# Kernel optimization log

Hardware: AMD Instinct MI355X
Metric: run time of the kernel (lower is better)

Reference implementation:

```python
import jax, jax.numpy as jnp
import numpy as np

HEADS = 16
DIM_HEAD = 64
SCALE = DIM_HEAD ** -0.5


def setup_inputs() -> dict:
    key = jax.random.key(0)
    k1, k2, k3 = jax.random.split(key, 3)
    B, N, C = 2, 2048, 1024
    inner = HEADS * DIM_HEAD  # 1024
    x = jax.random.normal(k1, (B, N, C), dtype=jnp.float32)
    w_qkv = jax.random.normal(k2, (C, 3 * inner), dtype=jnp.float32) * (C ** -0.5)
    w_proj = jax.random.normal(k3, (inner, C), dtype=jnp.float32) * (inner ** -0.5)
    b_proj = jnp.zeros((C,), dtype=jnp.float32)
    return {"x": x, "w_qkv": w_qkv, "w_proj": w_proj, "b_proj": b_proj}


def reference(x, w_qkv, w_proj, b_proj):
    B, N, C = x.shape
    qkv = x @ w_qkv  # [B, N, 3*inner]
    qkv = qkv.reshape(B, N, 3, HEADS, DIM_HEAD)
    qkv = jnp.transpose(qkv, (2, 0, 3, 1, 4))  # [3, B, H, N, D]
    q, k, v = qkv[0], qkv[1], qkv[2]
    q = q * SCALE
    attn = jnp.einsum('bhnd,bhmd->bhnm', q, k)  # [B, H, N, N]
    attn = jax.nn.softmax(attn, axis=-1)
    out = jnp.einsum('bhnm,bhmd->bhnd', attn, v)  # [B, H, N, D]
    out = jnp.transpose(out, (0, 2, 1, 3)).reshape(B, N, HEADS * DIM_HEAD)
    return out @ w_proj + b_proj
```

## Files before the change

### kernel.cpp

```cpp
#include <hip/hip_runtime.h>
#include <hip/hip_bf16.h>
#include <cstdint>
#include <cstddef>

static constexpr int BATCH = 2;
static constexpr int SEQ   = 2048;
static constexpr int CDIM  = 1024;
static constexpr int ROWS  = BATCH * SEQ;
static constexpr int QKVN  = 3 * CDIM;
static constexpr int QKN   = 2 * CDIM;

typedef short bf16x8 __attribute__((ext_vector_type(8)));
typedef short bf16x4 __attribute__((ext_vector_type(4)));
typedef float f32x4  __attribute__((ext_vector_type(4)));

__device__ inline short f2bf(float f) {
    union { float f; unsigned u; } v; v.f = f;
    unsigned u = v.u;
    u += 0x7fffu + ((u >> 16) & 1u);
    return (short)(u >> 16);
}

__device__ inline unsigned pk_bf16(float a, float b) {
#if __has_builtin(__builtin_amdgcn_cvt_pk_bf16_f32)
    auto r = __builtin_amdgcn_cvt_pk_bf16_f32(a, b);
    return __builtin_bit_cast(unsigned, r);
#else
    union { float f; unsigned u; } ua, ub;
    ua.f = a; ub.f = b;
    unsigned xa = ua.u + 0x7fffu + ((ua.u >> 16) & 1u);
    unsigned xb = ub.u + 0x7fffu + ((ub.u >> 16) & 1u);
    return __builtin_amdgcn_perm(xb, xa, 0x07060302);
#endif
}

__device__ inline void glds16(const short* g, short* l) {
    __builtin_amdgcn_global_load_lds(
        (const __attribute__((address_space(1))) void*)g,
        (__attribute__((address_space(3))) void*)l, 16, 0, 0);
}

__device__ inline f32x4 mfma16_bf16(bf16x4 a, bf16x4 b, f32x4 c) {
#if __has_builtin(__builtin_amdgcn_mfma_f32_16x16x16bf16_1k)
    return __builtin_amdgcn_mfma_f32_16x16x16bf16_1k(a, b, c, 0, 0, 0);
#else
    asm("v_mfma_f32_16x16x16_bf16 %0, %1, %2, %0" : "+v"(c) : "v"(a), "v"(b));
    return c;
#endif
}

__device__ inline int swz_src(int lane) {
    return ((lane & 3) ^ ((lane >> 3) & 3)) * 8;
}
__device__ inline int swz_rd(int quad, int l15) {
    return (quad ^ ((l15 >> 1) & 3)) * 8;
}

__global__ __launch_bounds__(256) void prep(const float* __restrict__ x,
                                            const float* __restrict__ wqkv,
                                            const float* __restrict__ wproj,
                                            short* __restrict__ x_bf,
                                            short* __restrict__ wqkvT,
                                            short* __restrict__ wprojT,
                                            float smul) {
    __shared__ float tile[32][33];
    const int bid = blockIdx.x, t = threadIdx.x;
    if (bid < 4096) {
        int i = bid * 256 + t;
        float4 f = ((const float4*)x)[i];
        uint2 o;
        o.x = pk_bf16(f.x, f.y);
        o.y = pk_bf16(f.z, f.w);
        ((uint2*)x_bf)[i] = o;
        return;
    }
    const float* in; short* out; int C, r0, c0; float scale; int srows;
    if (bid < 7168) {
        int b2 = bid - 4096;
        in = wqkv; out = wqkvT; C = QKVN;
        c0 = (b2 % 96) * 32; r0 = (b2 / 96) * 32;
        scale = smul; srows = 1024;
    } else {
        int b3 = bid - 7168;
        in = wproj; out = wprojT; C = CDIM;
        c0 = (b3 & 31) * 32; r0 = (b3 >> 5) * 32;
        scale = 1.0f; srows = 0;
    }
    int tx = t & 31, ty = t >> 5;
    #pragma unroll
    for (int i = 0; i < 4; i++)
        tile[ty + i * 8][tx] = in[(size_t)(r0 + ty + i * 8) * C + c0 + tx];
    __syncthreads();
    #pragma unroll
    for (int i = 0; i < 4; i++) {
        int orow = c0 + ty + i * 8;
        float sc = (orow < srows) ? scale : 1.0f;
        out[(size_t)orow * CDIM + r0 + tx] = f2bf(tile[tx][ty + i * 8] * sc);
    }
}

template<int BF16OUT, int MT>
__device__ __forceinline__ void gemm_core(const short* __restrict__ A,
                                          const short* __restrict__ Bt,
                                          void* __restrict__ C,
                                          const float* __restrict__ bias,
                                          int N, int K, int m0, int n0,
                                          short* As, short* Bs) {
    constexpr int AF = MT / 32;
    constexpr int APAN = MT * 32;
    constexpr int BPAN = 128 * 32;
    const int t = threadIdx.x, wave = t >> 6, lane = t & 63;
    const int l15 = lane & 15, quad = lane >> 4;
    const int wr = wave >> 1, wc = wave & 1;
    const int sg = swz_src(lane);
    const int rsl = swz_rd(quad, l15);

    f32x4 acc[AF][4] = {};

    const short* gA = A  + (size_t)(m0 + wave * (MT / 4) + (lane >> 2)) * K + sg;
    const short* gB = Bt + (size_t)(n0 + wave * 32 + (lane >> 2)) * K + sg;
    short* lA = &As[wave * (MT / 4) * 32];
    short* lB = &Bs[wave * 32 * 32];

    for (int k0 = 0; k0 < K; k0 += 64) {
        glds16(gA + k0,      lA);
        glds16(gA + k0 + 32, lA + APAN);
        if constexpr (MT == 128) {
            glds16(gA + 16 * K + k0,      lA + 512);
            glds16(gA + 16 * K + k0 + 32, lA + APAN + 512);
        }
        glds16(gB + k0,               lB);
        glds16(gB + 16 * K + k0,      lB + 512);
        glds16(gB + k0 + 32,          lB + BPAN);
        glds16(gB + 16 * K + k0 + 32, lB + BPAN + 512);
        __syncthreads();

        #pragma unroll
        for (int st = 0; st < 2; st++) {
            bf16x8 af[AF], bfv[4];
            #pragma unroll
            for (int i = 0; i < AF; i++)
                af[i] = *(const bf16x8*)&As[st * APAN + (wr * (MT / 2) + i * 16 + l15) * 32 + rsl];
            #pragma unroll
            for (int j = 0; j < 4; j++)
                bfv[j] = *(const bf16x8*)&Bs[st * BPAN + (wc * 64 + j * 16 + l15) * 32 + rsl];
            #pragma unroll
            for (int i = 0; i < AF; i++)
                #pragma unroll
                for (int j = 0; j < 4; j++)
                    acc[i][j] = __builtin_amdgcn_mfma_f32_16x16x32_bf16(af[i], bfv[j], acc[i][j], 0, 0, 0);
        }
        __syncthreads();
    }

    #pragma unroll
    for (int i = 0; i < AF; i++) {
        #pragma unroll
        for (int j = 0; j < 4; j++) {
            #pragma unroll
            for (int r = 0; r < 4; r++) {
                int row = m0 + wr * (MT / 2) + i * 16 + quad * 4 + r;
                int col = n0 + wc * 64 + j * 16 + l15;
                float v = acc[i][j][r];
                if (BF16OUT) ((short*)C)[(size_t)row * N + col] = f2bf(v);
                else         ((float*)C)[(size_t)row * N + col] = v + bias[col];
            }
        }
    }
}

__global__ __launch_bounds__(256) void gemm_qk_v(const short* __restrict__ x_bf,
                                                 const short* __restrict__ wqkvT,
                                                 short* __restrict__ qk,
                                                 short* __restrict__ vT) {
    __shared__ __align__(16) short As[128 * 64];
    __shared__ __align__(16) short Bs[128 * 64];
    const int bid = blockIdx.x;
    if (bid < 512) {
        gemm_core<1, 128>(x_bf, wqkvT, qk, nullptr, QKN, CDIM,
                          (bid >> 4) * 128, (bid & 15) * 128, As, Bs);
    } else {
        int b2 = bid - 512;
        gemm_core<1, 128>(wqkvT + (size_t)QKN * CDIM, x_bf, vT, nullptr, ROWS, CDIM,
                          (b2 >> 5) * 128, (b2 & 31) * 128, As, Bs);
    }
}

__global__ __launch_bounds__(256) void gemm_proj(const short* __restrict__ A,
                                                 const short* __restrict__ Bt,
                                                 float* __restrict__ C,
                                                 const float* __restrict__ bias) {
    __shared__ __align__(16) short As[64 * 64];
    __shared__ __align__(16) short Bs[128 * 64];
    gemm_core<0, 64>(A, Bt, C, bias, CDIM, CDIM,
                     blockIdx.y * 64, blockIdx.x * 128, As, Bs);
}

static constexpr int KBUF  = 2 * 128 * 32;
static constexpr int VOFF  = 2 * KBUF;
static constexpr int LDV   = 136;
static constexpr int VBUF  = 64 * LDV;
static constexpr int SMEM_SH = VOFF + 2 * VBUF;

__global__ __launch_bounds__(512) void attn_kernel(const short* __restrict__ qk,
                                                   const short* __restrict__ vTg,
                                                   short* __restrict__ attn_out) {
    __shared__ __align__(16) short smem[SMEM_SH];

    const int t = threadIdx.x, wave = t >> 6, lane = t & 63;
    const int l15 = lane & 15, quad = lane >> 4;
    const int g = wave >> 2, wl = wave & 3;
    const int lid = blockIdx.x;
    const int bh = (lid & 7) * 4 + (lid >> 7);
    const int q0 = ((lid >> 3) & 15) * 128;
    const int b = bh >> 4, h = bh & 15;
    const size_t baseQ = (size_t)(b * SEQ) * QKN + h * 64;
    const int rsl = swz_rd(quad, l15);

    const size_t qoff0 = baseQ + (size_t)(q0 + wl * 32 + l15) * QKN + quad * 8;
    const size_t qoff1 = qoff0 + (size_t)16 * QKN;
    bf16x8 qf00 = *(const bf16x8*)&qk[qoff0];
    bf16x8 qf01 = *(const bf16x8*)&qk[qoff0 + 32];
    bf16x8 qf10 = *(const bf16x8*)&qk[qoff1];
    bf16x8 qf11 = *(const bf16x8*)&qk[qoff1 + 32];

    const short* gK = qk + baseQ + 1024
                    + (size_t)(wave * 16 + (lane >> 2)) * QKN + swz_src(lane);
    const short* gV = vTg + (size_t)(h * 64) * ROWS + b * SEQ;
    const int vd = t >> 3, vc = t & 7;

    const bf16x4 ones = { (short)0x3F80, (short)0x3F80, (short)0x3F80, (short)0x3F80 };

    f32x4 ot0[4] = {}, ot1[4] = {};
    f32x4 ol0 = {}, ol1 = {};

    glds16(gK,      smem + wave * 512);
    glds16(gK + 32, smem + 4096 + wave * 512);
    {
        int4 va = *(const int4*)&gV[(size_t)vd * ROWS + vc * 8];
        int4 vb = *(const int4*)&gV[(size_t)vd * ROWS + 64 + vc * 8];
        *(int4*)&smem[VOFF + vd * LDV + vc * 8]      = va;
        *(int4*)&smem[VOFF + vd * LDV + 64 + vc * 8] = vb;
    }

    for (int j = 0; j < SEQ / 128; j++) {
        const int cur = j & 1, nxt = cur ^ 1;
        __syncthreads();

        int4 va, vb;
        if (j < SEQ / 128 - 1) {
            const size_t jadd = (size_t)(j + 1) * 128 * QKN;
            short* kb = smem + nxt * KBUF + wave * 512;
            glds16(gK + jadd,      kb);
            glds16(gK + jadd + 32, kb + 4096);
            va = *(const int4*)&gV[(size_t)vd * ROWS + (j + 1) * 128 + vc * 8];
            vb = *(const int4*)&gV[(size_t)vd * ROWS + (j + 1) * 128 + 64 + vc * 8];
        }

        const short* Kb0 = smem + cur * KBUF;
        const short* Kb1 = Kb0 + 4096;
        const short* Vb  = smem + VOFF + cur * VBUF;

        #pragma unroll
        for (int sub = 0; sub < 4; sub++) {
            const int gsub = g * 4 + sub;
            bf16x8 kf0 = *(const bf16x8*)&Kb0[(gsub * 16 + l15) * 32 + rsl];
            bf16x8 kf1 = *(const bf16x8*)&Kb1[(gsub * 16 + l15) * 32 + rsl];
            f32x4 a0 = {}, a1 = {};
            __builtin_amdgcn_s_setprio(1);
            a0 = __builtin_amdgcn_mfma_f32_16x16x32_bf16(kf0, qf00, a0, 0, 0, 0);
            a0 = __builtin_amdgcn_mfma_f32_16x16x32_bf16(kf1, qf01, a0, 0, 0, 0);
            a1 = __builtin_amdgcn_mfma_f32_16x16x32_bf16(kf0, qf10, a1, 0, 0, 0);
            a1 = __builtin_amdgcn_mfma_f32_16x16x32_bf16(kf1, qf11, a1, 0, 0, 0);
            __builtin_amdgcn_s_setprio(0);
            union { unsigned u[2]; bf16x4 v; } pu0, pu1;
            pu0.u[0] = pk_bf16(__builtin_amdgcn_exp2f(a0[0]), __builtin_amdgcn_exp2f(a0[1]));
            pu0.u[1] = pk_bf16(__builtin_amdgcn_exp2f(a0[2]), __builtin_amdgcn_exp2f(a0[3]));
            pu1.u[0] = pk_bf16(__builtin_amdgcn_exp2f(a1[0]), __builtin_amdgcn_exp2f(a1[1]));
            pu1.u[1] = pk_bf16(__builtin_amdgcn_exp2f(a1[2]), __builtin_amdgcn_exp2f(a1[3]));
            __builtin_amdgcn_s_setprio(1);
            ol0 = mfma16_bf16(ones, pu0.v, ol0);
            ol1 = mfma16_bf16(ones, pu1.v, ol1);
            #pragma unroll
            for (int d = 0; d < 4; d++) {
                bf16x4 vf = *(const bf16x4*)&Vb[(d * 16 + l15) * LDV + gsub * 16 + quad * 4];
                ot0[d] = mfma16_bf16(vf, pu0.v, ot0[d]);
                ot1[d] = mfma16_bf16(vf, pu1.v, ot1[d]);
            }
            __builtin_amdgcn_s_setprio(0);
        }

        if (j < SEQ / 128 - 1) {
            *(int4*)&smem[VOFF + nxt * VBUF + vd * LDV + vc * 8]      = va;
            *(int4*)&smem[VOFF + nxt * VBUF + vd * LDV + 64 + vc * 8] = vb;
        }
    }

    __syncthreads();
    float* pf   = (float*)smem;
    float* lbuf = (float*)smem + 128 * 68;
    short* tr   = smem + 18432;

    if (g == 1) {
        #pragma unroll
        for (int d = 0; d < 4; d++) {
            #pragma unroll
            for (int r = 0; r < 4; r++) {
                pf[(wl * 32 + l15) * 68      + d * 16 + quad * 4 + r] = ot0[d][r];
                pf[(wl * 32 + 16 + l15) * 68 + d * 16 + quad * 4 + r] = ot1[d][r];
            }
        }
        lbuf[wl * 32 + l15]      = ol0[0];
        lbuf[wl * 32 + 16 + l15] = ol1[0];
    }
    __syncthreads();
    if (g == 0) {
        float inv0 = 1.0f / (ol0[0] + lbuf[wl * 32 + l15]);
        float inv1 = 1.0f / (ol1[0] + lbuf[wl * 32 + 16 + l15]);
        #pragma unroll
        for (int d = 0; d < 4; d++) {
            int pb0 = (wl * 32 + l15) * 68      + d * 16 + quad * 4;
            int pb1 = (wl * 32 + 16 + l15) * 68 + d * 16 + quad * 4;
            float c00 = (ot0[d][0] + pf[pb0 + 0]) * inv0;
            float c01 = (ot0[d][1] + pf[pb0 + 1]) * inv0;
            float c02 = (ot0[d][2] + pf[pb0 + 2]) * inv0;
            float c03 = (ot0[d][3] + pf[pb0 + 3]) * inv0;
            float c10 = (ot1[d][0] + pf[pb1 + 0]) * inv1;
            float c11 = (ot1[d][1] + pf[pb1 + 1]) * inv1;
            float c12 = (ot1[d][2] + pf[pb1 + 2]) * inv1;
            float c13 = (ot1[d][3] + pf[pb1 + 3]) * inv1;
            int o0 = (wl * 32 + l15) * 72 + d * 16 + quad * 4;
            int o1 = (wl * 32 + 16 + l15) * 72 + d * 16 + quad * 4;
            *(unsigned*)&tr[o0]     = pk_bf16(c00, c01);
            *(unsigned*)&tr[o0 + 2] = pk_bf16(c02, c03);
            *(unsigned*)&tr[o1]     = pk_bf16(c10, c11);
            *(unsigned*)&tr[o1 + 2] = pk_bf16(c12, c13);
        }
    }
    __syncthreads();
    {
        int row = t >> 2, c4 = t & 3;
        #pragma unroll
        for (int p = 0; p < 2; p++) {
            int ch = c4 * 2 + p;
            int4 v = *(const int4*)&tr[row * 72 + ch * 8];
            *(int4*)&attn_out[(size_t)(b * SEQ + q0 + row) * CDIM + h * 64 + ch * 8] = v;
        }
    }
}

extern "C" void kernel_launch(void* const* d_in, const int* in_sizes, int n_in,
                              void* d_out, int out_size, void* d_ws, size_t ws_size,
                              hipStream_t stream) {
    const float* x      = (const float*)d_in[0];
    const float* w_qkv  = (const float*)d_in[1];
    const float* w_proj = (const float*)d_in[2];
    const float* b_proj = (const float*)d_in[3];
    float* out = (float*)d_out;

    char* ws = (char*)d_ws;
    short* x_bf    = (short*)(ws);
    short* wqkvT   = (short*)(ws + 8388608);
    short* wprojT  = (short*)(ws + 14680064);
    short* qk_bf   = (short*)(ws + 16777216);
    short* vTg     = (short*)(ws + 33554432);
    short* attn_bf = (short*)(ws + 41943040);

    const float SMUL = 0.125f * 1.44269504088896340736f;

    prep<<<8192, 256, 0, stream>>>(x, w_qkv, w_proj, x_bf, wqkvT, wprojT, SMUL);

    gemm_qk_v<<<768, 256, 0, stream>>>(x_bf, wqkvT, qk_bf, vTg);

    attn_kernel<<<dim3(512), 512, 0, stream>>>(qk_bf, vTg, attn_bf);

    gemm_proj<<<dim3(CDIM / 128, ROWS / 64), 256, 0, stream>>>(attn_bf, wprojT, out, b_proj);
}
```

Baseline: 181.6 us.

## Single-buffer V tile in LDS to shrink attention shared memory

Replaces the double-buffered V tile with a single V buffer and packs the epilogue scratch (row sums stored in a padding column of the partial-output buffer) so the kernel's shared memory drops to 26624 shorts. The intent is to fit more 512-thread blocks per CU and raise occupancy. In exchange, each iteration now needs an extra barrier before overwriting V and another after writing it, which adds synchronisation stalls and removes some of the overlap between the V store and compute.

```diff
diff --git a/kernel.cpp b/kernel.cpp
--- a/kernel.cpp
+++ b/kernel.cpp
@@ -200,7 +200,7 @@
 static constexpr int VOFF  = 2 * KBUF;
 static constexpr int LDV   = 136;
 static constexpr int VBUF  = 64 * LDV;
-static constexpr int SMEM_SH = VOFF + 2 * VBUF;
+static constexpr int SMEM_SH = 26624;
 
 __global__ __launch_bounds__(512) void attn_kernel(const short* __restrict__ qk,
                                                    const short* __restrict__ vTg,
@@ -234,32 +234,31 @@
     f32x4 ot0[4] = {}, ot1[4] = {};
     f32x4 ol0 = {}, ol1 = {};
 
+    short* Vbuf = smem + VOFF;
+
     glds16(gK,      smem + wave * 512);
     glds16(gK + 32, smem + 4096 + wave * 512);
     {
         int4 va = *(const int4*)&gV[(size_t)vd * ROWS + vc * 8];
         int4 vb = *(const int4*)&gV[(size_t)vd * ROWS + 64 + vc * 8];
-        *(int4*)&smem[VOFF + vd * LDV + vc * 8]      = va;
-        *(int4*)&smem[VOFF + vd * LDV + 64 + vc * 8] = vb;
-    }
+        *(int4*)&Vbuf[vd * LDV + vc * 8]      = va;
+        *(int4*)&Vbuf[vd * LDV + 64 + vc * 8] = vb;
+    }
+    __syncthreads();
 
     for (int j = 0; j < SEQ / 128; j++) {
-        const int cur = j & 1, nxt = cur ^ 1;
-        __syncthreads();
-
         int4 va, vb;
         if (j < SEQ / 128 - 1) {
             const size_t jadd = (size_t)(j + 1) * 128 * QKN;
-            short* kb = smem + nxt * KBUF + wave * 512;
+            short* kb = smem + ((j + 1) & 1) * KBUF + wave * 512;
             glds16(gK + jadd,      kb);
             glds16(gK + jadd + 32, kb + 4096);
             va = *(const int4*)&gV[(size_t)vd * ROWS + (j + 1) * 128 + vc * 8];
             vb = *(const int4*)&gV[(size_t)vd * ROWS + (j + 1) * 128 + 64 + vc * 8];
         }
 
-        const short* Kb0 = smem + cur * KBUF;
+        const short* Kb0 = smem + (j & 1) * KBUF;
         const short* Kb1 = Kb0 + 4096;
-        const short* Vb  = smem + VOFF + cur * VBUF;
 
         #pragma unroll
         for (int sub = 0; sub < 4; sub++) {
@@ -283,23 +282,24 @@
             ol1 = mfma16_bf16(ones, pu1.v, ol1);
             #pragma unroll
             for (int d = 0; d < 4; d++) {
-                bf16x4 vf = *(const bf16x4*)&Vb[(d * 16 + l15) * LDV + gsub * 16 + quad * 4];
+                bf16x4 vf = *(const bf16x4*)&Vbuf[(d * 16 + l15) * LDV + gsub * 16 + quad * 4];
                 ot0[d] = mfma16_bf16(vf, pu0.v, ot0[d]);
                 ot1[d] = mfma16_bf16(vf, pu1.v, ot1[d]);
             }
             __builtin_amdgcn_s_setprio(0);
         }
 
+        __syncthreads();
         if (j < SEQ / 128 - 1) {
-            *(int4*)&smem[VOFF + nxt * VBUF + vd * LDV + vc * 8]      = va;
-            *(int4*)&smem[VOFF + nxt * VBUF + vd * LDV + 64 + vc * 8] = vb;
-        }
-    }
-
-    __syncthreads();
-    float* pf   = (float*)smem;
-    float* lbuf = (float*)smem + 128 * 68;
-    short* tr   = smem + 18432;
+            *(int4*)&Vbuf[vd * LDV + vc * 8]      = va;
+            *(int4*)&Vbuf[vd * LDV + 64 + vc * 8] = vb;
+            __syncthreads();
+        }
+    }
+
+    __syncthreads();
+    float* pf = (float*)smem;
+    short* tr = smem + 17408;
 
     if (g == 1) {
         #pragma unroll
@@ -310,13 +310,13 @@
                 pf[(wl * 32 + 16 + l15) * 68 + d * 16 + quad * 4 + r] = ot1[d][r];
             }
         }
-        lbuf[wl * 32 + l15]      = ol0[0];
-        lbuf[wl * 32 + 16 + l15] = ol1[0];
+        pf[(wl * 32 + l15) * 68 + 64]      = ol0[0];
+        pf[(wl * 32 + 16 + l15) * 68 + 64] = ol1[0];
     }
     __syncthreads();
     if (g == 0) {
-        float inv0 = 1.0f / (ol0[0] + lbuf[wl * 32 + l15]);
-        float inv1 = 1.0f / (ol1[0] + lbuf[wl * 32 + 16 + l15]);
+        float inv0 = 1.0f / (ol0[0] + pf[(wl * 32 + l15) * 68 + 64]);
+        float inv1 = 1.0f / (ol1[0] + pf[(wl * 32 + 16 + l15) * 68 + 64]);
         #pragma unroll
         for (int d = 0; d < 4; d++) {
             int pb0 = (wl * 32 + l15) * 68      + d * 16 + quad * 4;
```

New measurement: 184.4 us. About the same (+1.6%).
